# Performance work log

Measured on AMD Instinct MI355X. Metric: run time of the kernel, lower is better.

Reference implementation:

```python
import jax, jax.numpy as jnp
import numpy as np
from jax import lax

P = 16      # n_features
H = 24      # hidden size (hard-coded in module)
B = 8192
T = 168


def setup_inputs() -> dict:
    key = jax.random.key(0)
    ks = jax.random.split(key, 8)
    s_ih = 1.0 / np.sqrt(H)
    return {
        "x": jax.random.normal(ks[0], (B, T, P), dtype=jnp.float32),
        # PyTorch LSTM params: gate order [i, f, g, o], uniform(-1/sqrt(H), 1/sqrt(H))
        "W_ih": jax.random.uniform(ks[1], (4 * H, P), jnp.float32, -s_ih, s_ih),
        "W_hh": jax.random.uniform(ks[2], (4 * H, H), jnp.float32, -s_ih, s_ih),
        "b_ih": jax.random.uniform(ks[3], (4 * H,), jnp.float32, -s_ih, s_ih),
        "b_hh": jax.random.uniform(ks[4], (4 * H,), jnp.float32, -s_ih, s_ih),
        "W_lin": jax.random.uniform(ks[5], (H, H), jnp.float32, -s_ih, s_ih),
        "b_lin": jax.random.uniform(ks[6], (H,), jnp.float32, -s_ih, s_ih),
    }


def _lstm_last_h(x, W_ih, W_hh, b_ih, b_hh):
    # Precompute input-side gate pre-activations for all timesteps: [B, T, 4H]
    xg = jnp.einsum("btp,gp->btg", x, W_ih) + (b_ih + b_hh)
    W_hh_T = W_hh.T  # [H, 4H]
    Bsz = x.shape[0]
    h0 = jnp.zeros((Bsz, H), dtype=x.dtype)
    c0 = jnp.zeros((Bsz, H), dtype=x.dtype)

    def step(carry, xt):
        h, c = carry
        g = xt + h @ W_hh_T  # [B, 4H]
        i = jax.nn.sigmoid(g[:, 0 * H:1 * H])
        f = jax.nn.sigmoid(g[:, 1 * H:2 * H])
        gg = jnp.tanh(g[:, 2 * H:3 * H])
        o = jax.nn.sigmoid(g[:, 3 * H:4 * H])
        c = f * c + i * gg
        h = o * jnp.tanh(c)
        return (h, c), None

    (h_last, _), _ = lax.scan(step, (h0, c0), jnp.swapaxes(xg, 0, 1))
    return h_last  # [B, H]


def reference(x, W_ih, W_hh, b_ih, b_hh, W_lin, b_lin):
    h_last = _lstm_last_h(x, W_ih, W_hh, b_ih, b_hh)
    # tanh over LSTM outputs, then linear head on the last timestep
    out = jnp.tanh(h_last) @ W_lin.T + b_lin  # [B, H]
    return out.reshape(out.shape[0], -1, 1)   # [B, 24, 1]
```

## Files before the change

### kernel.cpp

```cpp
#include <hip/hip_runtime.h>


#define T_STEPS 168
#define P_FEAT  16
#define TCH     84
#define NB      32
#define BPAD    24
#define BSTR    (TCH * 16 + BPAD)

typedef _Float16 half8 __attribute__((ext_vector_type(8)));
typedef _Float16 h2    __attribute__((ext_vector_type(2)));
typedef float    f32x4 __attribute__((ext_vector_type(4)));

__device__ __forceinline__ float rcp_fast(float x) {
#if __has_builtin(__builtin_amdgcn_rcpf)
    return __builtin_amdgcn_rcpf(x);
#else
    return 1.0f / x;
#endif
}
__device__ __forceinline__ float exp2_fast(float x) {
#if __has_builtin(__builtin_amdgcn_exp2f)
    return __builtin_amdgcn_exp2f(x);
#else
    return exp2f(x);
#endif
}
__device__ __forceinline__ float tanh_f(float x) {
    return 1.0f - 2.0f * rcp_fast(1.0f + exp2_fast(x * 2.88539008f));
}
__device__ __forceinline__ h2 pack2(float a, float b) {
    h2 r; r.x = (_Float16)a; r.y = (_Float16)b; return r;
}

__global__ __launch_bounds__(768, 3) void lstm_6t(
    const float* __restrict__ x,
    const float* __restrict__ W_ih,
    const float* __restrict__ W_hh,
    const float* __restrict__ b_ih,
    const float* __restrict__ b_hh,
    const float* __restrict__ W_lin,
    const float* __restrict__ b_lin,
    float* __restrict__ out)
{
    __shared__ __align__(16) _Float16 xs16[NB * BSTR];
    __shared__ __align__(16) _Float16 hx[2][2][4][16][8];
    __shared__ __align__(16) _Float16 zblk[16];
    __shared__ __align__(16) float    thbuf[2][16][25];

    const int tid  = threadIdx.x;
    const int w    = tid >> 6;
    const int lane = tid & 63;
    const int n    = lane & 15;
    const int q    = lane >> 4;
    const int cc   = (w >= 6);
    const int tau  = w - 6 * cc;
    const int batch = blockIdx.x * NB + 16 * cc + n;

    float* wstage = reinterpret_cast<float*>(xs16);
    for (int idx = tid; idx < 96 * 40; idx += 768) {
        const int j = idx / 40;
        const int k = idx - j * 40;
        wstage[idx] = (k < 24) ? W_hh[j * 24 + k] : W_ih[j * 16 + (k - 24)];
    }
    __syncthreads();

    half8 A1, A2;
    f32x4 biasf;
    {
        const int grow = (n & 3) * 24 + 6 * (n >> 2) + tau;
        #pragma unroll
        for (int j = 0; j < 8; j++) {
            A1[j] = (j < 6) ? (_Float16)wstage[grow * 40 + 6 * q + j] : (_Float16)0.0f;
            const int k = q * 8 + j;
            A2[j] = (k < 16) ? (_Float16)wstage[grow * 40 + 24 + k] : (_Float16)0.0f;
        }
        const int u = 6 * q + tau;
        #pragma unroll
        for (int r = 0; r < 4; r++)
            biasf[r] = b_ih[r * 24 + u] + b_hh[r * 24 + u];
    }
    {
        unsigned* hz = reinterpret_cast<unsigned*>(&hx[0][0][0][0][0]);
        if (tid < 512) { hz[tid] = 0u; hz[tid + 512] = 0u; }
        if (tid < 8) reinterpret_cast<unsigned*>(zblk)[tid] = 0u;
    }
    __syncthreads();

    float c  = 0.0f;
    float hv = 0.0f;

    const float4* xsrc = reinterpret_cast<const float4*>(x)
                       + (size_t)(blockIdx.x * NB) * (T_STEPS * P_FEAT / 4);

    const _Float16* xrowbase = (q < 2) ? &xs16[(16 * cc + n) * BSTR + q * 8] : zblk;
    const int xstep = (q < 2) ? 16 : 0;

    int bufp = 0;
    for (int ch = 0; ch < 2; ch++) {
        for (int i = 0; i < 14; i++) {
            const int m   = tid + 768 * i;
            const int b   = m / 336;
            const int rem = m - b * 336;
            const float4 v = xsrc[(size_t)b * 672 + ch * 336 + rem];
            h2* dst = reinterpret_cast<h2*>(xs16) + b * (BSTR / 2) + rem * 2;
            dst[0] = pack2(v.x, v.y);
            dst[1] = pack2(v.z, v.w);
        }
        __syncthreads();

        f32x4 gx;
        {
            const half8 B2 = *reinterpret_cast<const half8*>(xrowbase);
            gx = __builtin_amdgcn_mfma_f32_16x16x32_f16(A2, B2, biasf, 0, 0, 0);
        }

        for (int t = 0; t < TCH; t++) {
            const half8 B1 = *reinterpret_cast<const half8*>(&hx[bufp][cc][q][n][0]);
            const int tn = (t + 1 < TCH) ? t + 1 : 0;
            const half8 B2n = *reinterpret_cast<const half8*>(xrowbase + tn * xstep);

            f32x4 g = __builtin_amdgcn_mfma_f32_16x16x32_f16(A1, B1, gx, 0, 0, 0);
            gx = __builtin_amdgcn_mfma_f32_16x16x32_f16(A2, B2n, biasf, 0, 0, 0);

            {
                const float Y  = exp2_fast(g[0] * -1.44269504f);
                const float X  = exp2_fast(g[1] * -1.44269504f);
                const float Z  = exp2_fast(g[2] *  2.88539008f);
                const float V  = exp2_fast(g[3] * -1.44269504f);
                const float ax = 1.0f + X;
                const float ay = 1.0f + Y;
                const float az = 1.0f + Z;
                const float num = c * ay * az + ax * (Z - 1.0f);
                const float cn  = num * rcp_fast(ax * ay * az);
                c = cn;
                const float W  = exp2_fast(fminf(cn, 18.0f) * 2.88539008f);
                hv = (W - 1.0f) * rcp_fast((1.0f + V) * (1.0f + W));
            }

            hx[1 - bufp][cc][q][n][tau] = (_Float16)hv;
            bufp ^= 1;
            __syncthreads();
        }
    }

    thbuf[cc][n][6 * q + tau] = tanh_f(hv);
    __syncthreads();

    {
        const int u = 6 * q + tau;
        const float* wl = &W_lin[u * 24];
        float acc = b_lin[u];
        #pragma unroll
        for (int k = 0; k < 24; k++) acc = fmaf(thbuf[cc][n][k], wl[k], acc);
        out[(size_t)batch * 24 + u] = acc;
    }
}

extern "C" void kernel_launch(void* const* d_in, const int* in_sizes, int n_in,
                              void* d_out, int out_size, void* d_ws, size_t ws_size,
                              hipStream_t stream) {
    const float* x     = (const float*)d_in[0];
    const float* W_ih  = (const float*)d_in[1];
    const float* W_hh  = (const float*)d_in[2];
    const float* b_ih  = (const float*)d_in[3];
    const float* b_hh  = (const float*)d_in[4];
    const float* W_lin = (const float*)d_in[5];
    const float* b_lin = (const float*)d_in[6];
    float* out = (float*)d_out;

    const int B = in_sizes[0] / (T_STEPS * P_FEAT);
    dim3 grid(B / NB), block(768);
    lstm_6t<<<grid, block, 0, stream>>>(x, W_ih, W_hh, b_ih, b_hh, W_lin, b_lin, out);
}
```

Measured before the change: 194.5 us.

## Halve block to one 16-batch tile per block with lightweight LDS-only barrier

Each block now handles 16 sequences with 6 waves instead of 32 sequences with 12 waves, which doubles the grid and shrinks the per-step barrier to fewer waves. The per-timestep __syncthreads is replaced by an inline s_waitcnt lgkmcnt(0) plus s_barrier, so the step barrier no longer waits on outstanding global memory operations. The intent is to cut serial recurrence latency per step and let more independent blocks interleave on each CU. The cost is that weight staging and x loads are repeated across twice as many blocks, and each block has fewer waves to hide latency.

Result: slower. 199.7 us (+2.7%).

```diff
diff --git a/kernel.cpp b/kernel.cpp
--- a/kernel.cpp
+++ b/kernel.cpp
@@ -4,7 +4,7 @@
 #define T_STEPS 168
 #define P_FEAT  16
 #define TCH     84
-#define NB      32
+#define NB      16
 #define BPAD    24
 #define BSTR    (TCH * 16 + BPAD)
 
@@ -32,8 +32,11 @@
 __device__ __forceinline__ h2 pack2(float a, float b) {
     h2 r; r.x = (_Float16)a; r.y = (_Float16)b; return r;
 }
+__device__ __forceinline__ void soft_barrier() {
+    asm volatile("s_waitcnt lgkmcnt(0)\n\ts_barrier" ::: "memory");
+}
 
-__global__ __launch_bounds__(768, 3) void lstm_6t(
+__global__ __launch_bounds__(384, 3) void lstm_6w(
     const float* __restrict__ x,
     const float* __restrict__ W_ih,
     const float* __restrict__ W_hh,
@@ -44,21 +47,19 @@
     float* __restrict__ out)
 {
     __shared__ __align__(16) _Float16 xs16[NB * BSTR];
-    __shared__ __align__(16) _Float16 hx[2][2][4][16][8];
+    __shared__ __align__(16) _Float16 hx[2][4][16][8];
     __shared__ __align__(16) _Float16 zblk[16];
-    __shared__ __align__(16) float    thbuf[2][16][25];
+    __shared__ __align__(16) float    thbuf[16][25];
 
     const int tid  = threadIdx.x;
-    const int w    = tid >> 6;
+    const int tau  = tid >> 6;
     const int lane = tid & 63;
     const int n    = lane & 15;
     const int q    = lane >> 4;
-    const int cc   = (w >= 6);
-    const int tau  = w - 6 * cc;
-    const int batch = blockIdx.x * NB + 16 * cc + n;
+    const int batch = blockIdx.x * NB + n;
 
     float* wstage = reinterpret_cast<float*>(xs16);
-    for (int idx = tid; idx < 96 * 40; idx += 768) {
+    for (int idx = tid; idx < 96 * 40; idx += 384) {
         const int j = idx / 40;
         const int k = idx - j * 40;
         wstage[idx] = (k < 24) ? W_hh[j * 24 + k] : W_ih[j * 16 + (k - 24)];
@@ -81,8 +82,9 @@
             biasf[r] = b_ih[r * 24 + u] + b_hh[r * 24 + u];
     }
     {
-        unsigned* hz = reinterpret_cast<unsigned*>(&hx[0][0][0][0][0]);
-        if (tid < 512) { hz[tid] = 0u; hz[tid + 512] = 0u; }
+        unsigned* hz = reinterpret_cast<unsigned*>(&hx[0][0][0][0]);
+        hz[tid % 512] = 0u;
+        if (tid < 128) hz[384 + tid] = 0u;
         if (tid < 8) reinterpret_cast<unsigned*>(zblk)[tid] = 0u;
     }
     __syncthreads();
@@ -93,13 +95,13 @@
     const float4* xsrc = reinterpret_cast<const float4*>(x)
                        + (size_t)(blockIdx.x * NB) * (T_STEPS * P_FEAT / 4);
 
-    const _Float16* xrowbase = (q < 2) ? &xs16[(16 * cc + n) * BSTR + q * 8] : zblk;
+    const _Float16* xrowbase = (q < 2) ? &xs16[n * BSTR + q * 8] : zblk;
     const int xstep = (q < 2) ? 16 : 0;
 
     int bufp = 0;
     for (int ch = 0; ch < 2; ch++) {
         for (int i = 0; i < 14; i++) {
-            const int m   = tid + 768 * i;
+            const int m   = tid + 384 * i;
             const int b   = m / 336;
             const int rem = m - b * 336;
             const float4 v = xsrc[(size_t)b * 672 + ch * 336 + rem];
@@ -116,7 +118,7 @@
         }
 
         for (int t = 0; t < TCH; t++) {
-            const half8 B1 = *reinterpret_cast<const half8*>(&hx[bufp][cc][q][n][0]);
+            const half8 B1 = *reinterpret_cast<const half8*>(&hx[bufp][q][n][0]);
             const int tn = (t + 1 < TCH) ? t + 1 : 0;
             const half8 B2n = *reinterpret_cast<const half8*>(xrowbase + tn * xstep);
 
@@ -138,13 +140,13 @@
                 hv = (W - 1.0f) * rcp_fast((1.0f + V) * (1.0f + W));
             }
 
-            hx[1 - bufp][cc][q][n][tau] = (_Float16)hv;
+            hx[1 - bufp][q][n][tau] = (_Float16)hv;
             bufp ^= 1;
-            __syncthreads();
+            soft_barrier();
         }
     }
 
-    thbuf[cc][n][6 * q + tau] = tanh_f(hv);
+    thbuf[n][6 * q + tau] = tanh_f(hv);
     __syncthreads();
 
     {
@@ -152,7 +154,7 @@
         const float* wl = &W_lin[u * 24];
         float acc = b_lin[u];
         #pragma unroll
-        for (int k = 0; k < 24; k++) acc = fmaf(thbuf[cc][n][k], wl[k], acc);
+        for (int k = 0; k < 24; k++) acc = fmaf(thbuf[n][k], wl[k], acc);
         out[(size_t)batch * 24 + u] = acc;
     }
 }
@@ -170,6 +172,6 @@
     float* out = (float*)d_out;
 
     const int B = in_sizes[0] / (T_STEPS * P_FEAT);
-    dim3 grid(B / NB), block(768);
-    lstm_6t<<<grid, block, 0, stream>>>(x, W_ih, W_hh, b_ih, b_hh, W_lin, b_lin, out);
+    dim3 grid(B / NB), block(384);
+    lstm_6w<<<grid, block, 0, stream>>>(x, W_ih, W_hh, b_ih, b_hh, W_lin, b_lin, out);
 }
```
